# Performance work log

Measured on AMD Instinct MI355X. Metric: run time of the kernel, lower is better.

The kernel has to match this reference:

```python
import jax, jax.numpy as jnp
import numpy as np

B, A, T, D = 8, 50, 256, 128
HEADS, C = 32, 4  # C = D // HEADS
NEG_SLOPE = 0.2   # PyG GATConv default negative_slope


def setup_inputs() -> dict:
    key = jax.random.key(0)
    k1, k2, k3, k4 = jax.random.split(key, 4)
    h = jax.random.normal(k1, (B, A, T, D), dtype=jnp.float32)
    # PyG Linear weight [heads*out, in], applied as x @ W.T
    W = jax.random.normal(k2, (HEADS * C, D), dtype=jnp.float32) * (1.0 / np.sqrt(D))
    att_src = jax.random.normal(k3, (HEADS, C), dtype=jnp.float32) * 0.1
    att_dst = jax.random.normal(k4, (HEADS, C), dtype=jnp.float32) * 0.1
    bias = jnp.zeros((HEADS * C,), dtype=jnp.float32)
    return {"h": h, "W": W, "att_src": att_src, "att_dst": att_dst, "bias": bias}


def reference(h, W, att_src, att_dst, bias):
    # Graph is fully-connected-minus-self over A agents, replicated B*T times.
    # Equivalent dense form: per-destination softmax over all sources j != i.
    Bv, Av, Tv, Dv = h.shape
    x = h.transpose(0, 2, 1, 3).reshape(Bv * Tv, Av, Dv)          # [N, A, D], N = B*T graphs
    x = jnp.einsum('nad,ed->nae', x, W).reshape(Bv * Tv, Av, HEADS, C)  # W x, per head
    a_src = jnp.einsum('nahc,hc->nah', x, att_src)                # alpha_src[j]
    a_dst = jnp.einsum('nahc,hc->nah', x, att_dst)                # alpha_dst[i]
    # edge (j -> i): e_ij = leaky_relu(alpha_src[j] + alpha_dst[i])
    e = a_dst[:, :, None, :] + a_src[:, None, :, :]               # [N, i, j, H]
    e = jnp.where(e > 0, e, NEG_SLOPE * e)
    diag = jnp.eye(Av, dtype=bool)[None, :, :, None]              # no self-loops
    e = jnp.where(diag, -jnp.inf, e)
    alpha = jax.nn.softmax(e, axis=2)                             # scatter-softmax over src per dst
    out = jnp.einsum('nijh,njhc->nihc', alpha, x)                 # scatter-add aggregation
    out = out.reshape(Bv * Tv, Av, HEADS * C) + bias              # concat heads + bias
    return out.reshape(Bv, Tv, Av, HEADS * C).transpose(0, 2, 1, 3)  # (B, A, T, D)
```

## Files before the change

### kernel.cpp

```cpp
#include <hip/hip_runtime.h>
#include <hip/hip_bf16.h>

#define LOG2E 1.4426950408889634f

typedef __attribute__((ext_vector_type(8))) short bf16x8;
typedef __attribute__((ext_vector_type(4))) float f32x4;

static __device__ __forceinline__ float fast_exp2(float x) {
    return __builtin_amdgcn_exp2f(x);
}

static __device__ __forceinline__ short bf16bits(float f) {
    __hip_bfloat16 b = __float2bfloat16(f);
    return *reinterpret_cast<short*>(&b);
}

__global__ __launch_bounds__(256, 3) void gat_fused(
    const float* __restrict__ hsrc,
    const float* __restrict__ W,
    const float* __restrict__ att_src,
    const float* __restrict__ att_dst,
    const float* __restrict__ bias,
    float* __restrict__ out)
{
    constexpr int A = 50, T = 256, D = 128, H = 32;
    constexpr int XSS = 132;
    __shared__ __align__(16) char smem[64 * 128 * 2 + A * XSS * 4];
    short* hsb = (short*)smem;
    float* xs  = (float*)(smem + 64 * 128 * 2);
    float* asc = (float*)smem;
    float* ads = (float*)(smem + 6400);

    const int n = blockIdx.x;
    const int b = n >> 8;
    const int t = n & 255;
    const int tid = threadIdx.x;

    const float4* hg4 = (const float4*)hsrc;
    for (int idx = tid; idx < 64 * 32; idx += 256) {
        const int a = idx >> 5, k4 = idx & 31;
        short4 pk = {0, 0, 0, 0};
        if (a < A) {
            const float4 hv = hg4[((size_t)(b * A + a) * T + t) * 32 + k4];
            pk.x = bf16bits(hv.x); pk.y = bf16bits(hv.y);
            pk.z = bf16bits(hv.z); pk.w = bf16bits(hv.w);
        }
        const int swz = (k4 >> 1) ^ (a & 7);
        *(short4*)&hsb[a * 128 + swz * 8 + (k4 & 1) * 4] = pk;
    }
    __syncthreads();

    {
        const int wv = tid >> 6;
        const int lane = tid & 63;
        const int lr = lane & 15, lg = lane >> 4;
        const int n0 = wv * 32;
        f32x4 acc[4][2];
        #pragma unroll
        for (int m = 0; m < 4; ++m) {
            acc[m][0] = (f32x4){0.f, 0.f, 0.f, 0.f};
            acc[m][1] = (f32x4){0.f, 0.f, 0.f, 0.f};
        }
        const float4* W4 = (const float4*)W;
        #pragma unroll
        for (int kk = 0; kk < 4; ++kk) {
            const int kb = kk * 8 + lg * 2;
            const float4 wa = W4[(size_t)(n0 + lr) * 32 + kb];
            const float4 wb = W4[(size_t)(n0 + lr) * 32 + kb + 1];
            const float4 wc = W4[(size_t)(n0 + 16 + lr) * 32 + kb];
            const float4 wd = W4[(size_t)(n0 + 16 + lr) * 32 + kb + 1];
            bf16x8 bf0, bf1;
            bf0[0] = bf16bits(wa.x); bf0[1] = bf16bits(wa.y);
            bf0[2] = bf16bits(wa.z); bf0[3] = bf16bits(wa.w);
            bf0[4] = bf16bits(wb.x); bf0[5] = bf16bits(wb.y);
            bf0[6] = bf16bits(wb.z); bf0[7] = bf16bits(wb.w);
            bf1[0] = bf16bits(wc.x); bf1[1] = bf16bits(wc.y);
            bf1[2] = bf16bits(wc.z); bf1[3] = bf16bits(wc.w);
            bf1[4] = bf16bits(wd.x); bf1[5] = bf16bits(wd.y);
            bf1[6] = bf16bits(wd.z); bf1[7] = bf16bits(wd.w);
            #pragma unroll
            for (int m = 0; m < 4; ++m) {
                const int row = m * 16 + lr;
                const int chunk = (kk * 4 + lg) ^ (row & 7);
                const bf16x8 af = *(const bf16x8*)&hsb[row * 128 + chunk * 8];
                acc[m][0] = __builtin_amdgcn_mfma_f32_16x16x32_bf16(af, bf0, acc[m][0], 0, 0, 0);
                acc[m][1] = __builtin_amdgcn_mfma_f32_16x16x32_bf16(af, bf1, acc[m][1], 0, 0, 0);
            }
        }
        #pragma unroll
        for (int m = 0; m < 4; ++m) {
            const int rb = m * 16 + lg * 4;
            #pragma unroll
            for (int nt = 0; nt < 2; ++nt) {
                const int col = n0 + nt * 16 + lr;
                #pragma unroll
                for (int r = 0; r < 4; ++r) {
                    if (rb + r < A) xs[(rb + r) * XSS + col] = acc[m][nt][r];
                }
            }
        }
    }
    __syncthreads();

    for (int idx = tid; idx < A * H; idx += 256) {
        const int hh = idx & 31, a = idx >> 5;
        const float4 xv = *(const float4*)&xs[a * XSS + hh * 4];
        const float4 s4 = ((const float4*)att_src)[hh];
        const float4 d4 = ((const float4*)att_dst)[hh];
        asc[idx] = LOG2E * fmaf(xv.w, s4.w, fmaf(xv.z, s4.z, fmaf(xv.y, s4.y, xv.x * s4.x)));
        ads[idx] = LOG2E * fmaf(xv.w, d4.w, fmaf(xv.z, d4.z, fmaf(xv.y, d4.y, xv.x * d4.x)));
    }
    __syncthreads();

    {
        const int hh = tid & 31;
        const int ib = tid >> 5;
        float4 accv[7];
        float l[7], ad[7];
        #pragma unroll
        for (int r = 0; r < 7; ++r) {
            const int i = ib + 8 * r;
            const int ii = (i < A) ? i : (A - 1);
            ad[r] = ads[ii * H + hh];
            accv[r] = float4{0.f, 0.f, 0.f, 0.f};
            l[r] = 0.f;
        }
        #pragma unroll 5
        for (int j = 0; j < A; ++j) {
            const float as = asc[j * H + hh];
            const float4 xv = *(const float4*)&xs[j * XSS + hh * 4];
            #pragma unroll
            for (int r = 0; r < 7; ++r) {
                const float tt = ad[r] + as;
                const float ee = fmaxf(tt, 0.2f * tt);
                const float p  = fast_exp2(ee);
                l[r] += p;
                accv[r].x = fmaf(p, xv.x, accv[r].x);
                accv[r].y = fmaf(p, xv.y, accv[r].y);
                accv[r].z = fmaf(p, xv.z, accv[r].z);
                accv[r].w = fmaf(p, xv.w, accv[r].w);
            }
        }
        const float4 bv = ((const float4*)bias)[hh];
        #pragma unroll
        for (int r = 0; r < 7; ++r) {
            const int i = ib + 8 * r;
            if (i < A) {
                const float as = asc[i * H + hh];
                const float4 xv = *(const float4*)&xs[i * XSS + hh * 4];
                const float tt = ad[r] + as;
                const float ee = fmaxf(tt, 0.2f * tt);
                const float p  = fast_exp2(ee);
                const float linv = 1.0f / (l[r] - p);
                float4 o;
                o.x = fmaf(accv[r].x - p * xv.x, linv, bv.x);
                o.y = fmaf(accv[r].y - p * xv.y, linv, bv.y);
                o.z = fmaf(accv[r].z - p * xv.z, linv, bv.z);
                o.w = fmaf(accv[r].w - p * xv.w, linv, bv.w);
                *(float4*)&out[((size_t)(b * A + i) * T + t) * D + hh * 4] = o;
            }
        }
    }
}

extern "C" void kernel_launch(void* const* d_in, const int* in_sizes, int n_in,
                              void* d_out, int out_size, void* d_ws, size_t ws_size,
                              hipStream_t stream) {
    const float* h       = (const float*)d_in[0];
    const float* W       = (const float*)d_in[1];
    const float* att_src = (const float*)d_in[2];
    const float* att_dst = (const float*)d_in[3];
    const float* bias    = (const float*)d_in[4];
    float* out = (float*)d_out;
    dim3 grid(8 * 256);
    dim3 block(256);
    hipLaunchKernelGGL(gat_fused, grid, block, 0, stream,
                       h, W, att_src, att_dst, bias, out);
}
```

Before: 64.69 us.

## Factor exp of leaky-relu into precomputed exponentials and pre-convert W to bf16

The inner softmax loop no longer computes an exp per (i,j,head). It precomputes exp2(s) and exp2(0.2s) for the source and destination scores and forms p as max(Ed*Es, Fd*Fs), which works because exp is monotone. The accumulation is also rewritten with packed 2-wide float FMAs. A separate small kernel converts W to bf16 in the workspace, so each block loads bf16 fragments instead of converting fp32 weights itself. The factored exponentials can overflow or underflow for large scores, and the change adds an extra kernel launch.

```diff
diff --git a/kernel.cpp b/kernel.cpp
--- a/kernel.cpp
+++ b/kernel.cpp
@@ -5,6 +5,7 @@
 
 typedef __attribute__((ext_vector_type(8))) short bf16x8;
 typedef __attribute__((ext_vector_type(4))) float f32x4;
+typedef __attribute__((ext_vector_type(2))) float v2f;
 
 static __device__ __forceinline__ float fast_exp2(float x) {
     return __builtin_amdgcn_exp2f(x);
@@ -15,9 +16,16 @@
     return *reinterpret_cast<short*>(&b);
 }
 
+__global__ void wconv(const float* __restrict__ W, short* __restrict__ Wb) {
+    const int i = blockIdx.x * 256 + threadIdx.x;
+    Wb[i] = bf16bits(W[i]);
+}
+
+template<bool PRE>
 __global__ __launch_bounds__(256, 3) void gat_fused(
     const float* __restrict__ hsrc,
     const float* __restrict__ W,
+    const short* __restrict__ Wb,
     const float* __restrict__ att_src,
     const float* __restrict__ att_dst,
     const float* __restrict__ bias,
@@ -25,11 +33,11 @@
 {
     constexpr int A = 50, T = 256, D = 128, H = 32;
     constexpr int XSS = 132;
-    __shared__ __align__(16) char smem[64 * 128 * 2 + A * XSS * 4];
-    short* hsb = (short*)smem;
-    float* xs  = (float*)(smem + 64 * 128 * 2);
-    float* asc = (float*)smem;
-    float* ads = (float*)(smem + 6400);
+    __shared__ __align__(16) char smem[25600 + A * XSS * 4];
+    v2f*   EsFs = (v2f*)smem;
+    v2f*   EdFd = (v2f*)(smem + 12800);
+    short* hsb  = (short*)smem;
+    float* xs   = (float*)(smem + 25600);
 
     const int n = blockIdx.x;
     const int b = n >> 8;
@@ -61,23 +69,29 @@
             acc[m][0] = (f32x4){0.f, 0.f, 0.f, 0.f};
             acc[m][1] = (f32x4){0.f, 0.f, 0.f, 0.f};
         }
-        const float4* W4 = (const float4*)W;
         #pragma unroll
         for (int kk = 0; kk < 4; ++kk) {
-            const int kb = kk * 8 + lg * 2;
-            const float4 wa = W4[(size_t)(n0 + lr) * 32 + kb];
-            const float4 wb = W4[(size_t)(n0 + lr) * 32 + kb + 1];
-            const float4 wc = W4[(size_t)(n0 + 16 + lr) * 32 + kb];
-            const float4 wd = W4[(size_t)(n0 + 16 + lr) * 32 + kb + 1];
             bf16x8 bf0, bf1;
-            bf0[0] = bf16bits(wa.x); bf0[1] = bf16bits(wa.y);
-            bf0[2] = bf16bits(wa.z); bf0[3] = bf16bits(wa.w);
-            bf0[4] = bf16bits(wb.x); bf0[5] = bf16bits(wb.y);
-            bf0[6] = bf16bits(wb.z); bf0[7] = bf16bits(wb.w);
-            bf1[0] = bf16bits(wc.x); bf1[1] = bf16bits(wc.y);
-            bf1[2] = bf16bits(wc.z); bf1[3] = bf16bits(wc.w);
-            bf1[4] = bf16bits(wd.x); bf1[5] = bf16bits(wd.y);
-            bf1[6] = bf16bits(wd.z); bf1[7] = bf16bits(wd.w);
+            if (PRE) {
+                const bf16x8* Wb8 = (const bf16x8*)Wb;
+                bf0 = Wb8[(size_t)(n0 + lr) * 16 + kk * 4 + lg];
+                bf1 = Wb8[(size_t)(n0 + 16 + lr) * 16 + kk * 4 + lg];
+            } else {
+                const float4* W4 = (const float4*)W;
+                const int kb = kk * 8 + lg * 2;
+                const float4 wa = W4[(size_t)(n0 + lr) * 32 + kb];
+                const float4 wb = W4[(size_t)(n0 + lr) * 32 + kb + 1];
+                const float4 wc = W4[(size_t)(n0 + 16 + lr) * 32 + kb];
+                const float4 wd = W4[(size_t)(n0 + 16 + lr) * 32 + kb + 1];
+                bf0[0] = bf16bits(wa.x); bf0[1] = bf16bits(wa.y);
+                bf0[2] = bf16bits(wa.z); bf0[3] = bf16bits(wa.w);
+                bf0[4] = bf16bits(wb.x); bf0[5] = bf16bits(wb.y);
+                bf0[6] = bf16bits(wb.z); bf0[7] = bf16bits(wb.w);
+                bf1[0] = bf16bits(wc.x); bf1[1] = bf16bits(wc.y);
+                bf1[2] = bf16bits(wc.z); bf1[3] = bf16bits(wc.w);
+                bf1[4] = bf16bits(wd.x); bf1[5] = bf16bits(wd.y);
+                bf1[6] = bf16bits(wd.z); bf1[7] = bf16bits(wd.w);
+            }
             #pragma unroll
             for (int m = 0; m < 4; ++m) {
                 const int row = m * 16 + lr;
@@ -107,38 +121,41 @@
         const float4 xv = *(const float4*)&xs[a * XSS + hh * 4];
         const float4 s4 = ((const float4*)att_src)[hh];
         const float4 d4 = ((const float4*)att_dst)[hh];
-        asc[idx] = LOG2E * fmaf(xv.w, s4.w, fmaf(xv.z, s4.z, fmaf(xv.y, s4.y, xv.x * s4.x)));
-        ads[idx] = LOG2E * fmaf(xv.w, d4.w, fmaf(xv.z, d4.z, fmaf(xv.y, d4.y, xv.x * d4.x)));
+        const float asc = LOG2E * fmaf(xv.w, s4.w, fmaf(xv.z, s4.z, fmaf(xv.y, s4.y, xv.x * s4.x)));
+        const float ads = LOG2E * fmaf(xv.w, d4.w, fmaf(xv.z, d4.z, fmaf(xv.y, d4.y, xv.x * d4.x)));
+        EsFs[idx] = (v2f){fast_exp2(asc), fast_exp2(0.2f * asc)};
+        EdFd[idx] = (v2f){fast_exp2(ads), fast_exp2(0.2f * ads)};
     }
     __syncthreads();
 
     {
         const int hh = tid & 31;
         const int ib = tid >> 5;
-        float4 accv[7];
-        float l[7], ad[7];
+        v2f acc01[7], acc23[7], df[7];
+        float l[7];
         #pragma unroll
         for (int r = 0; r < 7; ++r) {
             const int i = ib + 8 * r;
             const int ii = (i < A) ? i : (A - 1);
-            ad[r] = ads[ii * H + hh];
-            accv[r] = float4{0.f, 0.f, 0.f, 0.f};
+            df[r] = EdFd[ii * H + hh];
+            acc01[r] = (v2f){0.f, 0.f};
+            acc23[r] = (v2f){0.f, 0.f};
             l[r] = 0.f;
         }
         #pragma unroll 5
         for (int j = 0; j < A; ++j) {
-            const float as = asc[j * H + hh];
+            const v2f sf = EsFs[j * H + hh];
             const float4 xv = *(const float4*)&xs[j * XSS + hh * 4];
+            const v2f x01 = (v2f){xv.x, xv.y};
+            const v2f x23 = (v2f){xv.z, xv.w};
             #pragma unroll
             for (int r = 0; r < 7; ++r) {
-                const float tt = ad[r] + as;
-                const float ee = fmaxf(tt, 0.2f * tt);
-                const float p  = fast_exp2(ee);
+                const v2f pe = df[r] * sf;
+                const float p = fmaxf(pe.x, pe.y);
                 l[r] += p;
-                accv[r].x = fmaf(p, xv.x, accv[r].x);
-                accv[r].y = fmaf(p, xv.y, accv[r].y);
-                accv[r].z = fmaf(p, xv.z, accv[r].z);
-                accv[r].w = fmaf(p, xv.w, accv[r].w);
+                const v2f pp = (v2f){p, p};
+                acc01[r] = __builtin_elementwise_fma(pp, x01, acc01[r]);
+                acc23[r] = __builtin_elementwise_fma(pp, x23, acc23[r]);
             }
         }
         const float4 bv = ((const float4*)bias)[hh];
@@ -146,17 +163,16 @@
         for (int r = 0; r < 7; ++r) {
             const int i = ib + 8 * r;
             if (i < A) {
-                const float as = asc[i * H + hh];
+                const v2f sf = EsFs[i * H + hh];
                 const float4 xv = *(const float4*)&xs[i * XSS + hh * 4];
-                const float tt = ad[r] + as;
-                const float ee = fmaxf(tt, 0.2f * tt);
-                const float p  = fast_exp2(ee);
+                const v2f pe = df[r] * sf;
+                const float p = fmaxf(pe.x, pe.y);
                 const float linv = 1.0f / (l[r] - p);
                 float4 o;
-                o.x = fmaf(accv[r].x - p * xv.x, linv, bv.x);
-                o.y = fmaf(accv[r].y - p * xv.y, linv, bv.y);
-                o.z = fmaf(accv[r].z - p * xv.z, linv, bv.z);
-                o.w = fmaf(accv[r].w - p * xv.w, linv, bv.w);
+                o.x = fmaf(acc01[r].x - p * xv.x, linv, bv.x);
+                o.y = fmaf(acc01[r].y - p * xv.y, linv, bv.y);
+                o.z = fmaf(acc23[r].x - p * xv.z, linv, bv.z);
+                o.w = fmaf(acc23[r].y - p * xv.w, linv, bv.w);
                 *(float4*)&out[((size_t)(b * A + i) * T + t) * D + hh * 4] = o;
             }
         }
@@ -174,6 +190,13 @@
     float* out = (float*)d_out;
     dim3 grid(8 * 256);
     dim3 block(256);
-    hipLaunchKernelGGL(gat_fused, grid, block, 0, stream,
-                       h, W, att_src, att_dst, bias, out);
-}
+    if (ws_size >= 128 * 128 * sizeof(short)) {
+        short* Wb = (short*)d_ws;
+        hipLaunchKernelGGL(wconv, dim3(64), block, 0, stream, W, Wb);
+        hipLaunchKernelGGL(gat_fused<true>, grid, block, 0, stream,
+                           h, W, Wb, att_src, att_dst, bias, out);
+    } else {
+        hipLaunchKernelGGL(gat_fused<false>, grid, block, 0, stream,
+                           h, W, (const short*)nullptr, att_src, att_dst, bias, out);
+    }
+}
```

New measurement: 57.75 us. 1.12x faster.
